# Kernel tuning notes

Hardware: AMD Instinct MI355X
Metric: run time of the kernel (lower is better)

The kernel has to match this reference:

```python
import jax, jax.numpy as jnp
import numpy as np

B, N, H = 2, 2048, 1024
NUM_HEADS, HEAD_DIM = 16, 64
SCALE = HEAD_DIM ** -0.5


def setup_inputs() -> dict:
    key = jax.random.key(0)
    ks = jax.random.split(key, 9)
    hidden_states = jax.random.normal(ks[0], (B, N, H), dtype=jnp.float32)
    # ancestor-only mask: lower-triangular incl. diagonal (chain tree)
    tree_mask = jnp.tril(jnp.ones((N, N), dtype=jnp.int32))
    s = H ** -0.5
    Wq = jax.random.normal(ks[1], (H, NUM_HEADS * HEAD_DIM), dtype=jnp.float32) * s
    Wk = jax.random.normal(ks[2], (H, NUM_HEADS * HEAD_DIM), dtype=jnp.float32) * s
    Wv = jax.random.normal(ks[3], (H, NUM_HEADS * HEAD_DIM), dtype=jnp.float32) * s
    Wo = jax.random.normal(ks[4], (NUM_HEADS * HEAD_DIM, H), dtype=jnp.float32) * s
    bq = jnp.zeros((NUM_HEADS * HEAD_DIM,), dtype=jnp.float32)
    bk = jnp.zeros((NUM_HEADS * HEAD_DIM,), dtype=jnp.float32)
    bv = jnp.zeros((NUM_HEADS * HEAD_DIM,), dtype=jnp.float32)
    bo = jnp.zeros((H,), dtype=jnp.float32)
    return {"hidden_states": hidden_states, "tree_mask": tree_mask,
            "Wq": Wq, "bq": bq, "Wk": Wk, "bk": bk,
            "Wv": Wv, "bv": bv, "Wo": Wo, "bo": bo}


def reference(hidden_states, tree_mask, Wq, bq, Wk, bk, Wv, bv, Wo, bo):
    b, n, _ = hidden_states.shape
    q = (hidden_states @ Wq + bq).reshape(b, n, NUM_HEADS, HEAD_DIM)
    k = (hidden_states @ Wk + bk).reshape(b, n, NUM_HEADS, HEAD_DIM)
    v = (hidden_states @ Wv + bv).reshape(b, n, NUM_HEADS, HEAD_DIM)
    # scores: [b, heads, n, n]
    scores = jnp.einsum('bqhd,bkhd->bhqk', q, k) * SCALE
    neg_inf = jnp.finfo(scores.dtype).min
    scores = jnp.where(tree_mask[None, None, :, :] == 0, neg_inf, scores)
    attn = jax.nn.softmax(scores, axis=-1)  # dropout p=0.0 -> identity
    out = jnp.einsum('bhqk,bkhd->bqhd', attn, v).reshape(b, n, NUM_HEADS * HEAD_DIM)
    return out @ Wo + bo
```

## Files before the change

kernel.cpp:

```cpp
#include <hip/hip_runtime.h>
#include <hip/hip_bf16.h>
#include <stdint.h>

typedef unsigned short u16;
typedef short short8 __attribute__((ext_vector_type(8)));
typedef float f32x4 __attribute__((ext_vector_type(4)));
typedef u16 u16x4 __attribute__((ext_vector_type(4)));

#define SCLOG 0.18033688011112042f

static __device__ __forceinline__ u16 f2bf(float f) {
  unsigned u = __float_as_uint(f);
  unsigned rnd = 0x7fffu + ((u >> 16) & 1u);
  return (u16)((u + rnd) >> 16);
}

static __device__ __forceinline__ unsigned pk_bf16(float a, float b) {
  unsigned r;
  asm("v_cvt_pk_bf16_f32 %0, %1, %2" : "=v"(r) : "v"(a), "v"(b));
  return r;
}

static __device__ __forceinline__ void gload_lds16(const void* g, void* l) {
  __builtin_amdgcn_global_load_lds(
      (const __attribute__((address_space(1))) unsigned int*)g,
      (__attribute__((address_space(3))) unsigned int*)l, 16, 0, 0);
}

__global__ __launch_bounds__(256) void prep_kernel(
    const float* __restrict__ hs, const int* __restrict__ mask,
    const float* __restrict__ Wq, const float* __restrict__ Wk,
    const float* __restrict__ Wv, const float* __restrict__ Wo,
    u16* __restrict__ X, u16* __restrict__ WT,
    unsigned long long* __restrict__ bits) {
  __shared__ float tile[32][33];
  const int bid = blockIdx.x;
  const int tid = threadIdx.x;
  if (bid < 4096) {
    const int i = bid * 256 + tid;
    const float4 v = reinterpret_cast<const float4*>(hs)[i];
    u16x4 o;
    o[0] = f2bf(v.x); o[1] = f2bf(v.y); o[2] = f2bf(v.z); o[3] = f2bf(v.w);
    reinterpret_cast<u16x4*>(X)[i] = o;
  } else if (bid < 8192) {
    const int B = bid - 4096;
    const int z = B >> 10, y = (B >> 5) & 31, x = B & 31;
    const float* src = (z == 0) ? Wq : (z == 1) ? Wk : (z == 2) ? Wv : Wo;
    u16* dst = WT + (size_t)z * 1024 * 1024;
    const int row0 = y * 32, col0 = x * 32;
    const int tx = tid & 31, ty = tid >> 5;
#pragma unroll
    for (int i = 0; i < 4; ++i)
      tile[ty + i * 8][tx] = src[(size_t)(row0 + ty + i * 8) * 1024 + col0 + tx];
    __syncthreads();
#pragma unroll
    for (int i = 0; i < 4; ++i) {
      const int r = ty + i * 8;
      dst[(size_t)(col0 + r) * 1024 + row0 + tx] = f2bf(tile[tx][r]);
    }
  } else {
    const int gw = (bid - 8192) * 4 + (tid >> 6);
    const int lane = tid & 63;
    const int q = gw >> 5, w = gw & 31;
    const int mv = mask[(size_t)q * 2048 + w * 64 + lane];
    const unsigned long long bal = __ballot(mv != 0);
    if (lane == 0) bits[(size_t)q * 32 + w] = bal;
  }
}

__global__ __launch_bounds__(256) void gemm_qkv_kernel(
    const u16* __restrict__ X, const u16* __restrict__ WT,
    const float* __restrict__ bq, const float* __restrict__ bk, const float* __restrict__ bv,
    u16* __restrict__ Qb, u16* __restrict__ Kb, u16* __restrict__ Vb) {
  __shared__ u16 As[128 * 32];
  __shared__ u16 Bs[128 * 32];
  const int tid = threadIdx.x;
  const int lane = tid & 63, wid = tid >> 6;
  const int l15 = lane & 15, lg = lane >> 4;
  const int n0 = blockIdx.x * 128, m0 = blockIdx.y * 128;
  const int wr = wid >> 1, wc = wid & 1;

  f32x4 acc[4][4] = {};

  for (int kt = 0; kt < 32; ++kt) {
    __syncthreads();
#pragma unroll
    for (int p = 0; p < 2; ++p) {
      const int c = p * 256 + tid;
      const int r = c >> 2, ch = c & 3;
      gload_lds16(X + (size_t)(m0 + r) * 1024 + kt * 32 + ch * 8,
                  &As[(p * 256 + wid * 64) * 8]);
      gload_lds16(WT + (size_t)(n0 + r) * 1024 + kt * 32 + ch * 8,
                  &Bs[(p * 256 + wid * 64) * 8]);
    }
    __syncthreads();
    short8 af[4], bfr[4];
#pragma unroll
    for (int i = 0; i < 4; ++i) {
      af[i] = *reinterpret_cast<const short8*>(&As[(wr * 64 + i * 16 + l15) * 32 + lg * 8]);
      bfr[i] = *reinterpret_cast<const short8*>(&Bs[(wc * 64 + i * 16 + l15) * 32 + lg * 8]);
    }
#pragma unroll
    for (int i = 0; i < 4; ++i)
#pragma unroll
      for (int j = 0; j < 4; ++j)
        acc[i][j] = __builtin_amdgcn_mfma_f32_16x16x32_bf16(bfr[j], af[i], acc[i][j], 0, 0, 0);
  }

#pragma unroll
  for (int i = 0; i < 4; ++i) {
    const int m = m0 + wr * 64 + i * 16 + l15;
    const int bb = m >> 11, t = m & 2047;
#pragma unroll
    for (int j = 0; j < 4; ++j) {
      const int n = n0 + wc * 64 + j * 16 + lg * 4;
      const float* bsrc = (n < 1024) ? (bq + n) : (n < 2048) ? (bk + n - 1024) : (bv + n - 2048);
      const float4 b4 = *reinterpret_cast<const float4*>(bsrc);
      const float scl = (n < 1024) ? SCLOG : 1.0f;
      u16* dst = (n < 1024) ? Qb : (n < 2048) ? Kb : Vb;
      const int nl = n & 1023;
      const int hh = nl >> 6, d0 = nl & 63;
      uint2 pk;
      pk.x = pk_bf16((acc[i][j][0] + b4.x) * scl, (acc[i][j][1] + b4.y) * scl);
      pk.y = pk_bf16((acc[i][j][2] + b4.z) * scl, (acc[i][j][3] + b4.w) * scl);
      *reinterpret_cast<uint2*>(dst + ((size_t)(bb * 16 + hh) * 2048 + t) * 64 + d0) = pk;
    }
  }
}

__global__ __launch_bounds__(256) void transpose_v_kernel(const u16* __restrict__ Vb,
                                                          u16* __restrict__ VT) {
  __shared__ u16 tile[64][68];
  const int tid = threadIdx.x;
  const int tt = blockIdx.x & 31;
  const int bh = blockIdx.x >> 5;
  const size_t base = (size_t)bh * 2048 * 64;
  const int t0 = tt * 64;
#pragma unroll
  for (int p = 0; p < 2; ++p) {
    int i = p * 256 + tid;
    int row = i >> 3, ch = i & 7;
    *reinterpret_cast<short8*>(&tile[row][ch * 8]) =
        *reinterpret_cast<const short8*>(Vb + base + (size_t)(t0 + row) * 64 + ch * 8);
  }
  __syncthreads();
#pragma unroll
  for (int p = 0; p < 2; ++p) {
    int i = p * 256 + tid;
    int d = i >> 3, ch = i & 7;
    short8 v;
#pragma unroll
    for (int j = 0; j < 8; ++j) v[j] = tile[ch * 8 + j][d];
    *reinterpret_cast<short8*>(VT + base + (size_t)d * 2048 + t0 + ch * 8) = v;
  }
}

struct AttnState {
  f32x4 O[4];
  float m, l;
  short8 qf0, qf1;
};

static __device__ __forceinline__ void attn_tile(
    AttnState& st, const u16* __restrict__ Kb_, const u16* __restrict__ Vb_,
    u16* __restrict__ pwave, unsigned long long w,
    int l15, int lg, int slg) {
  f32x4 sT[4] = {};
  __builtin_amdgcn_s_setprio(1);
#pragma unroll
  for (int dc = 0; dc < 2; ++dc) {
    const short8 qv = dc ? st.qf1 : st.qf0;
#pragma unroll
    for (int sub = 0; sub < 4; ++sub) {
      const short8 kf = *reinterpret_cast<const short8*>(
          &Kb_[dc * 2048 + (sub * 16 + l15) * 32 + slg]);
      sT[sub] = __builtin_amdgcn_mfma_f32_16x16x32_bf16(kf, qv, sT[sub], 0, 0, 0);
    }
  }
  __builtin_amdgcn_s_setprio(0);

  float pm = -3e38f;
  if (__all(w == ~0ull)) {
#pragma unroll
    for (int sub = 0; sub < 4; ++sub)
#pragma unroll
      for (int r = 0; r < 4; ++r) pm = fmaxf(pm, sT[sub][r]);
  } else {
    const unsigned mlo = (unsigned)w, mhi = (unsigned)(w >> 32);
#pragma unroll
    for (int sub = 0; sub < 4; ++sub) {
      const unsigned f = ((sub & 2) ? mhi : mlo) >> ((sub & 1) * 16 + lg * 4);
#pragma unroll
      for (int r = 0; r < 4; ++r) {
        const float val = ((f >> r) & 1u) ? sT[sub][r] : -1e30f;
        sT[sub][r] = val;
        pm = fmaxf(pm, val);
      }
    }
  }
  pm = fmaxf(pm, __shfl_xor(pm, 16));
  pm = fmaxf(pm, __shfl_xor(pm, 32));
  if (!__all(pm - st.m <= 8.f)) {
    const float mn = fmaxf(st.m, pm);
    const float al = exp2f(st.m - mn);
    st.m = mn;
    st.l *= al;
#pragma unroll
    for (int dt = 0; dt < 4; ++dt) st.O[dt] *= al;
  }

  float lsum = 0.f;
#pragma unroll
  for (int kc = 0; kc < 2; ++kc) {
#pragma unroll
    for (int s2 = 0; s2 < 2; ++s2) {
      const int sub = kc * 2 + s2;
      const float e0 = exp2f(sT[sub][0] - st.m);
      const float e1 = exp2f(sT[sub][1] - st.m);
      const float e2 = exp2f(sT[sub][2] - st.m);
      const float e3 = exp2f(sT[sub][3] - st.m);
      lsum += (e0 + e1) + (e2 + e3);
      uint2 pk;
      pk.x = pk_bf16(e0, e1);
      pk.y = pk_bf16(e2, e3);
      *reinterpret_cast<uint2*>(&pwave[l15 * 40 + s2 * 16 + lg * 4]) = pk;
    }
    const short8 pf = *reinterpret_cast<const short8*>(&pwave[l15 * 40 + lg * 8]);
    __builtin_amdgcn_s_setprio(1);
#pragma unroll
    for (int dt = 0; dt < 4; ++dt) {
      const short8 vf = *reinterpret_cast<const short8*>(
          &Vb_[kc * 2048 + (dt * 16 + l15) * 32 + slg]);
      st.O[dt] = __builtin_amdgcn_mfma_f32_16x16x32_bf16(vf, pf, st.O[dt], 0, 0, 0);
    }
    __builtin_amdgcn_s_setprio(0);
  }
  lsum += __shfl_xor(lsum, 16);
  lsum += __shfl_xor(lsum, 32);
  st.l += lsum;
}

__global__ __launch_bounds__(256, 4) void attn_kernel(
    const u16* __restrict__ Q, const u16* __restrict__ K, const u16* __restrict__ VT,
    const unsigned long long* __restrict__ MB, u16* __restrict__ AO) {
  __shared__ u16 K_lds[2][4096];
  __shared__ u16 V_lds[2][4096];
  __shared__ u16 p_lds[4][16][40];
  __shared__ unsigned actA_s, actB_s;

  const int tid = threadIdx.x;
  const int wid = tid >> 6, lane = tid & 63;
  const int l15 = lane & 15, lg = lane >> 4;

  const int qp = blockIdx.x;
  const int qA_t = qp, qB_t = 31 - qp;
  const int h = blockIdx.y;
  const int b = blockIdx.z;
  const size_t bh_off = ((size_t)(b * 16 + h)) * 2048 * 64;

  if (tid == 0) { actA_s = 0; actB_s = 0; }
  __syncthreads();
  {
    const int ktc = tid & 31, qg = tid >> 5;
    unsigned long long orA = 0, orB = 0;
#pragma unroll
    for (int i = 0; i < 8; ++i) {
      orA |= MB[(size_t)(qA_t * 64 + qg * 8 + i) * 32 + ktc];
      orB |= MB[(size_t)(qB_t * 64 + qg * 8 + i) * 32 + ktc];
    }
    if (orA) atomicOr(&actA_s, 1u << ktc);
    if (orB) atomicOr(&actB_s, 1u << ktc);
  }

  const int qa = qA_t * 64 + wid * 16 + l15;
  const int qb = qB_t * 64 + wid * 16 + l15;

  AttnState stA, stB;
  {
    const short8* qpA = reinterpret_cast<const short8*>(Q + bh_off + (size_t)qa * 64);
    const short8* qpB = reinterpret_cast<const short8*>(Q + bh_off + (size_t)qb * 64);
    stA.qf0 = qpA[lg]; stA.qf1 = qpA[4 + lg];
    stB.qf0 = qpB[lg]; stB.qf1 = qpB[4 + lg];
#pragma unroll
    for (int dt = 0; dt < 4; ++dt) { stA.O[dt] = f32x4{}; stB.O[dt] = f32x4{}; }
    stA.m = -3e38f; stA.l = 0.f;
    stB.m = -3e38f; stB.l = 0.f;
  }

  const int slg = (lg ^ ((l15 >> 1) & 3)) * 8;

  int offK[2], offV[2], ldsi[2];
#pragma unroll
  for (int p = 0; p < 2; ++p) {
    const int i = wid * 128 + p * 64 + lane;
    const int pc = i >> 8, row = (i >> 2) & 63, lgc = i & 3;
    const int lgs = lgc ^ ((i >> 3) & 3);
    offK[p] = row * 64 + pc * 32 + lgs * 8;
    offV[p] = row * 2048 + pc * 32 + lgs * 8;
    ldsi[p] = (wid * 128 + p * 64) * 8;
  }
  const u16* Kg = K + bh_off;
  const u16* Vg = VT + bh_off;
  u16* pwave = &p_lds[wid][0][0];

  __syncthreads();
  const unsigned actA = actA_s, actB = actB_s;
  unsigned rem = actA | actB;
  int buf = 0;

#define STAGE_TILE(bb, ktv)                                        \
  do {                                                             \
    const u16* ksrc_ = Kg + (ktv) * 64 * 64;                       \
    const u16* vsrc_ = Vg + (ktv) * 64;                            \
    _Pragma("unroll") for (int p_ = 0; p_ < 2; ++p_) {             \
      gload_lds16(ksrc_ + offK[p_], &K_lds[bb][ldsi[p_]]);         \
      gload_lds16(vsrc_ + offV[p_], &V_lds[bb][ldsi[p_]]);         \
    }                                                              \
  } while (0)

  if (rem) {
    int kt = __ffs(rem) - 1;
    unsigned long long wA_cur = MB[(size_t)qa * 32 + kt];
    unsigned long long wB_cur = MB[(size_t)qb * 32 + kt];
    STAGE_TILE(0, kt);
    __syncthreads();

    while (true) {
      rem &= rem - 1;
      int ktn = -1;
      unsigned long long wA_next = 0, wB_next = 0;
      if (rem) {
        ktn = __ffs(rem) - 1;
        wA_next = MB[(size_t)qa * 32 + ktn];
        wB_next = MB[(size_t)qb * 32 + ktn];
        STAGE_TILE(buf ^ 1, ktn);
      }

      if ((actB >> kt) & 1u)
        attn_tile(stB, &K_lds[buf][0], &V_lds[buf][0], pwave, wB_cur, l15, lg, slg);
      if ((actA >> kt) & 1u)
        attn_tile(stA, &K_lds[buf][0], &V_lds[buf][0], pwave, wA_cur, l15, lg, slg);

      if (ktn < 0) break;
      __syncthreads();
      buf ^= 1;
      kt = ktn;
      wA_cur = wA_next;
      wB_cur = wB_next;
    }
  }
#undef STAGE_TILE

  {
    const float invA = (stA.l > 0.f) ? (1.0f / stA.l) : 0.f;
    u16* dstA = AO + ((size_t)(b * 2048 + qa)) * 1024 + h * 64;
#pragma unroll
    for (int dt = 0; dt < 4; ++dt) {
      uint2 pk;
      pk.x = pk_bf16(stA.O[dt][0] * invA, stA.O[dt][1] * invA);
      pk.y = pk_bf16(stA.O[dt][2] * invA, stA.O[dt][3] * invA);
      *reinterpret_cast<uint2*>(dstA + dt * 16 + lg * 4) = pk;
    }
    const float invB = (stB.l > 0.f) ? (1.0f / stB.l) : 0.f;
    u16* dstB = AO + ((size_t)(b * 2048 + qb)) * 1024 + h * 64;
#pragma unroll
    for (int dt = 0; dt < 4; ++dt) {
      uint2 pk;
      pk.x = pk_bf16(stB.O[dt][0] * invB, stB.O[dt][1] * invB);
      pk.y = pk_bf16(stB.O[dt][2] * invB, stB.O[dt][3] * invB);
      *reinterpret_cast<uint2*>(dstB + dt * 16 + lg * 4) = pk;
    }
  }
}

__global__ __launch_bounds__(256) void gemm_out_kernel(
    const u16* __restrict__ A, const u16* __restrict__ BT,
    const float* __restrict__ bo, float* __restrict__ out) {
  __shared__ u16 As[128 * 32];
  __shared__ u16 Bs[128 * 32];
  const int tid = threadIdx.x;
  const int lane = tid & 63, wid = tid >> 6;
  const int l15 = lane & 15, lg = lane >> 4;
  const int n0 = blockIdx.x * 128, m0 = blockIdx.y * 128;
  const int wr = wid >> 1, wc = wid & 1;

  f32x4 acc[4][4] = {};

  for (int kt = 0; kt < 32; ++kt) {
    __syncthreads();
#pragma unroll
    for (int p = 0; p < 2; ++p) {
      const int c = p * 256 + tid;
      const int r = c >> 2, ch = c & 3;
      gload_lds16(A + (size_t)(m0 + r) * 1024 + kt * 32 + ch * 8,
                  &As[(p * 256 + wid * 64) * 8]);
      gload_lds16(BT + (size_t)(n0 + r) * 1024 + kt * 32 + ch * 8,
                  &Bs[(p * 256 + wid * 64) * 8]);
    }
    __syncthreads();
    short8 af[4], bfr[4];
#pragma unroll
    for (int i = 0; i < 4; ++i) {
      af[i] = *reinterpret_cast<const short8*>(&As[(wr * 64 + i * 16 + l15) * 32 + lg * 8]);
      bfr[i] = *reinterpret_cast<const short8*>(&Bs[(wc * 64 + i * 16 + l15) * 32 + lg * 8]);
    }
#pragma unroll
    for (int i = 0; i < 4; ++i)
#pragma unroll
      for (int j = 0; j < 4; ++j)
        acc[i][j] = __builtin_amdgcn_mfma_f32_16x16x32_bf16(bfr[j], af[i], acc[i][j], 0, 0, 0);
  }

#pragma unroll
  for (int i = 0; i < 4; ++i) {
    const int m = m0 + wr * 64 + i * 16 + l15;
#pragma unroll
    for (int j = 0; j < 4; ++j) {
      const int n = n0 + wc * 64 + j * 16 + lg * 4;
      const float4 b4 = *reinterpret_cast<const float4*>(bo + n);
      float4 o4;
      o4.x = acc[i][j][0] + b4.x;
      o4.y = acc[i][j][1] + b4.y;
      o4.z = acc[i][j][2] + b4.z;
      o4.w = acc[i][j][3] + b4.w;
      *reinterpret_cast<float4*>(out + (size_t)m * 1024 + n) = o4;
    }
  }
}

extern "C" void kernel_launch(void* const* d_in, const int* in_sizes, int n_in,
                              void* d_out, int out_size, void* d_ws, size_t ws_size,
                              hipStream_t stream) {
  (void)in_sizes; (void)n_in; (void)out_size; (void)ws_size;
  const float* hs = (const float*)d_in[0];
  const int* mask = (const int*)d_in[1];
  const float* Wq = (const float*)d_in[2];
  const float* bq = (const float*)d_in[3];
  const float* Wk = (const float*)d_in[4];
  const float* bk = (const float*)d_in[5];
  const float* Wv = (const float*)d_in[6];
  const float* bv = (const float*)d_in[7];
  const float* Wo = (const float*)d_in[8];
  const float* bo = (const float*)d_in[9];
  float* out = (float*)d_out;

  uint8_t* ws = (uint8_t*)d_ws;
  u16* X  = (u16*)(ws);
  u16* WT = (u16*)(ws + ((size_t)8 << 20));
  u16* Qb = (u16*)(ws + ((size_t)16 << 20));
  u16* Kb = (u16*)(ws + ((size_t)24 << 20));
  u16* Vb = (u16*)(ws + ((size_t)32 << 20));
  u16* AO = (u16*)(ws + ((size_t)40 << 20));
  unsigned long long* MB = (unsigned long long*)(ws + ((size_t)48 << 20));
  u16* VbT = X;

  prep_kernel<<<dim3(24576), dim3(256), 0, stream>>>(hs, mask, Wq, Wk, Wv, Wo, X, WT, MB);
  gemm_qkv_kernel<<<dim3(24, 32), dim3(256), 0, stream>>>(X, WT, bq, bk, bv, Qb, Kb, Vb);
  transpose_v_kernel<<<dim3(1024), dim3(256), 0, stream>>>(Vb, VbT);
  attn_kernel<<<dim3(16, 16, 2), dim3(256), 0, stream>>>(Qb, Kb, VbT, MB, AO);
  gemm_out_kernel<<<dim3(8, 32), dim3(256), 0, stream>>>(AO, WT + (size_t)3072 * 1024, bo, out);
}
```

Before: 146.9 us.

## Split attention query tiles to 32 rows, one state per wave, XCD-aware grid

Attention work is reorganized so each workgroup handles two 32-row query tiles (a causal-balanced pair), with each pair of waves owning one tile and a single softmax state instead of two states per wave. The grid becomes a flat 1024-block launch with an index remap that groups heads/batches across XCDs. The row-sum cross-lane reduction is deferred to the epilogue, and the max reduction is rebalanced as a tree. This doubles block count and halves per-wave register state for better occupancy, at the cost of each K/V tile staged into LDS serving fewer query rows (more K/V reload traffic).

```diff
diff --git a/kernel.cpp b/kernel.cpp
--- a/kernel.cpp
+++ b/kernel.cpp
@@ -179,24 +179,23 @@
   }
   __builtin_amdgcn_s_setprio(0);
 
-  float pm = -3e38f;
-  if (__all(w == ~0ull)) {
-#pragma unroll
-    for (int sub = 0; sub < 4; ++sub)
-#pragma unroll
-      for (int r = 0; r < 4; ++r) pm = fmaxf(pm, sT[sub][r]);
-  } else {
+  if (!__all(w == ~0ull)) {
     const unsigned mlo = (unsigned)w, mhi = (unsigned)(w >> 32);
 #pragma unroll
     for (int sub = 0; sub < 4; ++sub) {
       const unsigned f = ((sub & 2) ? mhi : mlo) >> ((sub & 1) * 16 + lg * 4);
 #pragma unroll
-      for (int r = 0; r < 4; ++r) {
-        const float val = ((f >> r) & 1u) ? sT[sub][r] : -1e30f;
-        sT[sub][r] = val;
-        pm = fmaxf(pm, val);
-      }
-    }
+      for (int r = 0; r < 4; ++r)
+        sT[sub][r] = ((f >> r) & 1u) ? sT[sub][r] : -1e30f;
+    }
+  }
+  float pm;
+  {
+    const float t0 = fmaxf(fmaxf(sT[0][0], sT[0][1]), fmaxf(sT[0][2], sT[0][3]));
+    const float t1 = fmaxf(fmaxf(sT[1][0], sT[1][1]), fmaxf(sT[1][2], sT[1][3]));
+    const float t2 = fmaxf(fmaxf(sT[2][0], sT[2][1]), fmaxf(sT[2][2], sT[2][3]));
+    const float t3 = fmaxf(fmaxf(sT[3][0], sT[3][1]), fmaxf(sT[3][2], sT[3][3]));
+    pm = fmaxf(fmaxf(t0, t1), fmaxf(t2, t3));
   }
   pm = fmaxf(pm, __shfl_xor(pm, 16));
   pm = fmaxf(pm, __shfl_xor(pm, 32));
@@ -235,8 +234,6 @@
     }
     __builtin_amdgcn_s_setprio(0);
   }
-  lsum += __shfl_xor(lsum, 16);
-  lsum += __shfl_xor(lsum, 32);
   st.l += lsum;
 }
 
@@ -252,39 +249,39 @@
   const int wid = tid >> 6, lane = tid & 63;
   const int l15 = lane & 15, lg = lane >> 4;
 
-  const int qp = blockIdx.x;
-  const int qA_t = qp, qB_t = 31 - qp;
-  const int h = blockIdx.y;
-  const int b = blockIdx.z;
+  const int wgid = blockIdx.x;
+  const int x = wgid & 7, s = wgid >> 3;
+  const int g = x + 8 * (s >> 5);
+  const int qp = s & 31;
+  const int h = g & 15, b = g >> 4;
+  const int qA_t = qp, qB_t = 63 - qp;
   const size_t bh_off = ((size_t)(b * 16 + h)) * 2048 * 64;
 
   if (tid == 0) { actA_s = 0; actB_s = 0; }
   __syncthreads();
   {
-    const int ktc = tid & 31, qg = tid >> 5;
+    const int ktc = tid & 31, rg = tid >> 5;
     unsigned long long orA = 0, orB = 0;
 #pragma unroll
-    for (int i = 0; i < 8; ++i) {
-      orA |= MB[(size_t)(qA_t * 64 + qg * 8 + i) * 32 + ktc];
-      orB |= MB[(size_t)(qB_t * 64 + qg * 8 + i) * 32 + ktc];
+    for (int i = 0; i < 4; ++i) {
+      orA |= MB[(size_t)(qA_t * 32 + rg * 4 + i) * 32 + ktc];
+      orB |= MB[(size_t)(qB_t * 32 + rg * 4 + i) * 32 + ktc];
     }
     if (orA) atomicOr(&actA_s, 1u << ktc);
     if (orB) atomicOr(&actB_s, 1u << ktc);
   }
 
-  const int qa = qA_t * 64 + wid * 16 + l15;
-  const int qb = qB_t * 64 + wid * 16 + l15;
-
-  AttnState stA, stB;
+  const int sid = wid >> 1;
+  const int qt = sid ? qB_t : qA_t;
+  const int q = qt * 32 + (wid & 1) * 16 + l15;
+
+  AttnState st;
   {
-    const short8* qpA = reinterpret_cast<const short8*>(Q + bh_off + (size_t)qa * 64);
-    const short8* qpB = reinterpret_cast<const short8*>(Q + bh_off + (size_t)qb * 64);
-    stA.qf0 = qpA[lg]; stA.qf1 = qpA[4 + lg];
-    stB.qf0 = qpB[lg]; stB.qf1 = qpB[4 + lg];
-#pragma unroll
-    for (int dt = 0; dt < 4; ++dt) { stA.O[dt] = f32x4{}; stB.O[dt] = f32x4{}; }
-    stA.m = -3e38f; stA.l = 0.f;
-    stB.m = -3e38f; stB.l = 0.f;
+    const short8* qp_ = reinterpret_cast<const short8*>(Q + bh_off + (size_t)q * 64);
+    st.qf0 = qp_[lg]; st.qf1 = qp_[4 + lg];
+#pragma unroll
+    for (int dt = 0; dt < 4; ++dt) st.O[dt] = f32x4{};
+    st.m = -3e38f; st.l = 0.f;
   }
 
   const int slg = (lg ^ ((l15 >> 1) & 3)) * 8;
@@ -305,6 +302,7 @@
 
   __syncthreads();
   const unsigned actA = actA_s, actB = actB_s;
+  const unsigned actW = sid ? actB : actA;
   unsigned rem = actA | actB;
   int buf = 0;
 
@@ -320,55 +318,44 @@
 
   if (rem) {
     int kt = __ffs(rem) - 1;
-    unsigned long long wA_cur = MB[(size_t)qa * 32 + kt];
-    unsigned long long wB_cur = MB[(size_t)qb * 32 + kt];
+    unsigned long long w_cur = MB[(size_t)q * 32 + kt];
     STAGE_TILE(0, kt);
     __syncthreads();
 
     while (true) {
       rem &= rem - 1;
       int ktn = -1;
-      unsigned long long wA_next = 0, wB_next = 0;
+      unsigned long long w_next = 0;
       if (rem) {
         ktn = __ffs(rem) - 1;
-        wA_next = MB[(size_t)qa * 32 + ktn];
-        wB_next = MB[(size_t)qb * 32 + ktn];
+        w_next = MB[(size_t)q * 32 + ktn];
         STAGE_TILE(buf ^ 1, ktn);
       }
 
-      if ((actB >> kt) & 1u)
-        attn_tile(stB, &K_lds[buf][0], &V_lds[buf][0], pwave, wB_cur, l15, lg, slg);
-      if ((actA >> kt) & 1u)
-        attn_tile(stA, &K_lds[buf][0], &V_lds[buf][0], pwave, wA_cur, l15, lg, slg);
+      if ((actW >> kt) & 1u)
+        attn_tile(st, &K_lds[buf][0], &V_lds[buf][0], pwave, w_cur, l15, lg, slg);
 
       if (ktn < 0) break;
       __syncthreads();
       buf ^= 1;
       kt = ktn;
-      wA_cur = wA_next;
-      wB_cur = wB_next;
+      w_cur = w_next;
     }
   }
 #undef STAGE_TILE
 
   {
-    const float invA = (stA.l > 0.f) ? (1.0f / stA.l) : 0.f;
-    u16* dstA = AO + ((size_t)(b * 2048 + qa)) * 1024 + h * 64;
+    float lr = st.l;
+    lr += __shfl_xor(lr, 16);
+    lr += __shfl_xor(lr, 32);
+    const float inv = (lr > 0.f) ? (1.0f / lr) : 0.f;
+    u16* dst = AO + ((size_t)(b * 2048 + q)) * 1024 + h * 64;
 #pragma unroll
     for (int dt = 0; dt < 4; ++dt) {
       uint2 pk;
-      pk.x = pk_bf16(stA.O[dt][0] * invA, stA.O[dt][1] * invA);
-      pk.y = pk_bf16(stA.O[dt][2] * invA, stA.O[dt][3] * invA);
-      *reinterpret_cast<uint2*>(dstA + dt * 16 + lg * 4) = pk;
-    }
-    const float invB = (stB.l > 0.f) ? (1.0f / stB.l) : 0.f;
-    u16* dstB = AO + ((size_t)(b * 2048 + qb)) * 1024 + h * 64;
-#pragma unroll
-    for (int dt = 0; dt < 4; ++dt) {
-      uint2 pk;
-      pk.x = pk_bf16(stB.O[dt][0] * invB, stB.O[dt][1] * invB);
-      pk.y = pk_bf16(stB.O[dt][2] * invB, stB.O[dt][3] * invB);
-      *reinterpret_cast<uint2*>(dstB + dt * 16 + lg * 4) = pk;
+      pk.x = pk_bf16(st.O[dt][0] * inv, st.O[dt][1] * inv);
+      pk.y = pk_bf16(st.O[dt][2] * inv, st.O[dt][3] * inv);
+      *reinterpret_cast<uint2*>(dst + dt * 16 + lg * 4) = pk;
     }
   }
 }
@@ -457,6 +444,6 @@
   prep_kernel<<<dim3(24576), dim3(256), 0, stream>>>(hs, mask, Wq, Wk, Wv, Wo, X, WT, MB);
   gemm_qkv_kernel<<<dim3(24, 32), dim3(256), 0, stream>>>(X, WT, bq, bk, bv, Qb, Kb, Vb);
   transpose_v_kernel<<<dim3(1024), dim3(256), 0, stream>>>(Vb, VbT);
-  attn_kernel<<<dim3(16, 16, 2), dim3(256), 0, stream>>>(Qb, Kb, VbT, MB, AO);
+  attn_kernel<<<dim3(1024), dim3(256), 0, stream>>>(Qb, Kb, VbT, MB, AO);
   gemm_out_kernel<<<dim3(8, 32), dim3(256), 0, stream>>>(AO, WT + (size_t)3072 * 1024, bo, out);
 }
```

Measured after the change: 143.6 us. -2.2%, faster.
